# Kernel optimization log

Hardware: AMD Instinct MI355X
Metric: run time of the kernel (lower is better)

## Reference

```python
import jax, jax.numpy as jnp
import numpy as np

N_E = 1024
E_DIM = 64
BETA = 0.25


def setup_inputs() -> dict:
    key = jax.random.key(0)
    k1, k2 = jax.random.split(key)
    z = jax.random.normal(k1, (16, E_DIM, 64, 64), dtype=jnp.float32)
    # torch init: uniform(-1/n_e, 1/n_e)
    emb_w = jax.random.uniform(k2, (N_E, E_DIM), dtype=jnp.float32,
                               minval=-1.0 / N_E, maxval=1.0 / N_E)
    return {"z": z, "emb_w": emb_w}


def reference(z, emb_w):
    bt, ch, h, w = z.shape
    # (B, C, H, W) -> (B, H, W, C) -> (N, e_dim)
    z_perm = jnp.transpose(z, (0, 2, 3, 1))
    z_flat = z_perm.reshape(-1, ch)  # (N, e_dim)

    # squared euclidean distances: (N, n_e)
    distances = (jnp.sum(z_flat ** 2, axis=1, keepdims=True)
                 + jnp.sum(emb_w ** 2, axis=1)
                 - 2.0 * jnp.matmul(z_flat, emb_w.T))
    min_idx = jnp.argmin(distances, axis=1)  # (N,)

    min_encodings = jax.nn.one_hot(min_idx, N_E, dtype=z.dtype)  # (N, n_e)

    # gather codebook vectors (same math as one_hot @ emb_w)
    z_q = emb_w[min_idx].reshape(bt, h, w, ch)
    z_q = jnp.transpose(z_q, (0, 3, 1, 2))  # (B, C, H, W)

    commitment_loss = BETA * jnp.mean((jax.lax.stop_gradient(z_q) - z) ** 2)
    loss = commitment_loss

    # straight-through estimator
    z_q_st = z + jax.lax.stop_gradient(z_q - z)

    avg_probs = jnp.mean(min_encodings, axis=0)
    perplexity = jnp.exp(-jnp.sum(avg_probs * jnp.log(avg_probs + 1e-10)))

    min_encoding_indices = min_idx.reshape(bt, h, w)
    return loss, z_q_st, perplexity, min_encodings, min_encoding_indices
```

## Files before the change

### kernel.cpp

```cpp
#include <hip/hip_runtime.h>
#include <math.h>

#define NPOS   65536
#define NE     1024
#define EDIM   64
#define HW     4096
#define BETA   0.25

#define OUT_LOSS 0LL
#define OUT_ZQ   1LL
#define OUT_PERP 4194305LL
#define OUT_ENC  4194306LL
#define OUT_IDX  71303170LL

#define POSB 128
#define JT   128

__device__ __forceinline__ float pairwise_sum_sq64(const float v[64]) {
#pragma clang fp contract(off)
    float r[8];
#pragma unroll
    for (int k = 0; k < 8; ++k) r[k] = v[k] * v[k];
#pragma unroll
    for (int i = 8; i < 64; i += 8) {
#pragma unroll
        for (int k = 0; k < 8; ++k) {
            float s = v[i + k] * v[i + k];
            r[k] = r[k] + s;
        }
    }
    return ((r[0] + r[1]) + (r[2] + r[3])) + ((r[4] + r[5]) + (r[6] + r[7]));
}

__global__ void vq_prep(const float* __restrict__ emb, float* __restrict__ enorm,
                        float* __restrict__ embT, int* __restrict__ counts,
                        double* __restrict__ lacc) {
    int t = blockIdx.x * 256 + threadIdx.x;
    if (t < NE) {
        float v[64];
#pragma unroll
        for (int c = 0; c < 64; ++c) v[c] = emb[t * 64 + c];
        enorm[t] = pairwise_sum_sq64(v);
#pragma unroll
        for (int c = 0; c < 64; ++c) embT[c * NE + t] = v[c];
        counts[t] = 0;
    }
    if (t == 0) *lacc = 0.0;
}

__global__ __launch_bounds__(256, 4)
void vq_main(const float* __restrict__ z, const float* __restrict__ emb,
             const float* __restrict__ embT, const float* __restrict__ enorm,
             int* __restrict__ counts, double* __restrict__ lacc,
             float* __restrict__ out) {
    __shared__ float z_lds[64 * POSB];
    __shared__ float e_lds[64 * JT];
    __shared__ float enorm_lds[NE];
    __shared__ float szn_lds[POSB];
    __shared__ float run_d[POSB];
    __shared__ int   run_j[POSB];

    const int tid   = threadIdx.x;
    const int tpos  = tid >> 4;
    const int tcode = tid & 15;
    const int n0    = blockIdx.x * POSB;
    const int b     = n0 >> 12;
    const int hw0   = n0 & 4095;
    const int zbase = b * (64 * HW) + hw0;

#pragma unroll
    for (int it = 0; it < 8; ++it) {
        const int idx4 = it * 256 + tid;
        const int c    = idx4 >> 5;
        const int p4   = idx4 & 31;
        const float4 v = *(const float4*)(z + zbase + c * HW + p4 * 4);
        *(float4*)(&z_lds[c * POSB + p4 * 4]) = v;
    }
#pragma unroll
    for (int it = 0; it < 4; ++it) enorm_lds[it * 256 + tid] = enorm[it * 256 + tid];
    if (tid < POSB) { run_d[tid] = 3.4e38f; run_j[tid] = 0; }
    __syncthreads();

    if (tid < POSB) {
#pragma clang fp contract(off)
        float r[8];
#pragma unroll
        for (int k = 0; k < 8; ++k) { float x = z_lds[k * POSB + tid]; r[k] = x * x; }
#pragma unroll
        for (int i = 8; i < 64; i += 8) {
#pragma unroll
            for (int k = 0; k < 8; ++k) {
                float x = z_lds[(i + k) * POSB + tid];
                float s = x * x;
                r[k] = r[k] + s;
            }
        }
        szn_lds[tid] = ((r[0] + r[1]) + (r[2] + r[3])) + ((r[4] + r[5]) + (r[6] + r[7]));
    }
    __syncthreads();

    for (int jo = 0; jo < 8; ++jo) {
        const int j0 = jo * JT;

#pragma unroll
        for (int it = 0; it < 8; ++it) {
            const int idx4 = it * 256 + tid;
            const int c    = idx4 >> 5;
            const int q4   = idx4 & 31;
            const float4 v = *(const float4*)(embT + c * NE + j0 + q4 * 4);
            *(float4*)(&e_lds[c * JT + q4 * 4]) = v;
        }
        __syncthreads();

        float acc[8][8];
#pragma unroll
        for (int i = 0; i < 8; ++i)
#pragma unroll
            for (int u = 0; u < 8; ++u) acc[i][u] = 0.0f;

#pragma unroll 2
        for (int c = 0; c < 64; ++c) {
            const float4 za = *(const float4*)(&z_lds[c * POSB + tpos * 8]);
            const float4 zb = *(const float4*)(&z_lds[c * POSB + tpos * 8 + 4]);
            const float4 ea = *(const float4*)(&e_lds[c * JT + tcode * 4]);
            const float4 eb = *(const float4*)(&e_lds[c * JT + 64 + tcode * 4]);
            const float zf[8] = {za.x, za.y, za.z, za.w, zb.x, zb.y, zb.z, zb.w};
            const float ef[8] = {ea.x, ea.y, ea.z, ea.w, eb.x, eb.y, eb.z, eb.w};
#pragma unroll
            for (int i = 0; i < 8; ++i)
#pragma unroll
                for (int u = 0; u < 8; ++u)
                    acc[i][u] = fmaf(zf[i], ef[u], acc[i][u]);
        }

#pragma unroll
        for (int i = 0; i < 8; ++i) {
            const int p = tpos * 8 + i;
            const float sz = szn_lds[p];
            float bd = 3.4e38f;
            int   bj = 0;
#pragma unroll
            for (int u = 0; u < 4; ++u) {
                const int j = j0 + tcode * 4 + u;
                const float dj = (sz + enorm_lds[j]) - 2.0f * acc[i][u];
                if (dj < bd) { bd = dj; bj = j; }
            }
#pragma unroll
            for (int u = 0; u < 4; ++u) {
                const int j = j0 + 64 + tcode * 4 + u;
                const float dj = (sz + enorm_lds[j]) - 2.0f * acc[i][4 + u];
                if (dj < bd) { bd = dj; bj = j; }
            }
#pragma unroll
            for (int m = 1; m < 16; m <<= 1) {
                const float od = __shfl_xor(bd, m, 64);
                const int   oj = __shfl_xor(bj, m, 64);
                if (od < bd || (od == bd && oj < bj)) { bd = od; bj = oj; }
            }
            if (tcode == 0) {
                if (bd < run_d[p]) { run_d[p] = bd; run_j[p] = bj; }
            }
        }
        __syncthreads();
    }

    if (tid < POSB) {
        const int j = run_j[tid];
        atomicAdd(&counts[j], 1);
        out[OUT_IDX + n0 + tid] = (float)j;
        out[OUT_ENC + (long long)(n0 + tid) * NE + j] = 1.0f;
    }

    {
        const int pos = tid & 127;
        const int half = tid >> 7;
        const int myj = run_j[pos];
        double acc2 = 0.0;
#pragma unroll
        for (int k = 0; k < 32; ++k) {
            const int c = half * 32 + k;
            const float zc = z_lds[c * POSB + pos];
            const float ec = emb[myj * 64 + c];
            const float t  = __fsub_rn(ec, zc);
            const float o  = __fadd_rn(zc, t);
            out[OUT_ZQ + (long long)b * (64LL * HW) + (long long)c * HW + hw0 + pos] = o;
            const float s = __fmul_rn(t, t);
            acc2 += (double)s;
        }
#pragma unroll
        for (int off = 32; off > 0; off >>= 1) acc2 += __shfl_down(acc2, off);
        if ((tid & 63) == 0) atomicAdd(lacc, acc2);
    }
}

__global__ void vq_finalize(const int* __restrict__ counts,
                            const double* __restrict__ lacc,
                            float* __restrict__ out) {
    __shared__ float red[1024];
    const int t = threadIdx.x;
    const float p = (float)counts[t] * (1.0f / 65536.0f);
    const float term = p * logf(p + 1e-10f);
    red[t] = term;
    __syncthreads();
    for (int s = 512; s > 0; s >>= 1) {
        if (t < s) red[t] += red[t + s];
        __syncthreads();
    }
    if (t == 0) {
        out[OUT_PERP] = expf(-red[0]);
        out[OUT_LOSS] = (float)(BETA * (*lacc / 4194304.0));
    }
}

extern "C" void kernel_launch(void* const* d_in, const int* in_sizes, int n_in,
                              void* d_out, int out_size, void* d_ws, size_t ws_size,
                              hipStream_t stream) {
    const float* z   = (const float*)d_in[0];
    const float* emb = (const float*)d_in[1];
    float* out = (float*)d_out;

    double* lacc  = (double*)d_ws;
    int*    cnts  = (int*)((char*)d_ws + 16);
    float*  enorm = (float*)((char*)d_ws + 16 + NE * sizeof(int));
    float*  embT  = (float*)((char*)d_ws + 16 + NE * sizeof(int) + NE * sizeof(float));

    hipMemsetAsync(out + OUT_ENC, 0, (size_t)NPOS * NE * sizeof(float), stream);

    vq_prep<<<4, 256, 0, stream>>>(emb, enorm, embT, cnts, lacc);
    vq_main<<<512, 256, 0, stream>>>(z, emb, embT, enorm, cnts, lacc, out);
    vq_finalize<<<1, 1024, 0, stream>>>(cnts, lacc, out);
}
```

Measured before the change: 202.5 us.

## Fuse one-hot encoding write into main kernel and enlarge per-thread register tile

Drops the separate memset of the 256MB one-hot output and has the main kernel write every one-hot row directly, with zeros and the single one together as float2 stores. Block size is halved to 128 threads and each thread now handles 16 positions by 8 codes, keeping running minima and position norms in registers instead of LDS. This removes one full pass over the large output and some LDS traffic. In exchange the one-hot writes are serialized over 128 rows per block, and register pressure is higher with a single block allowed per CU by the launch bounds, which may cut occupancy.

```diff
diff --git a/kernel.cpp b/kernel.cpp
--- a/kernel.cpp
+++ b/kernel.cpp
@@ -48,7 +48,7 @@
     if (t == 0) *lacc = 0.0;
 }
 
-__global__ __launch_bounds__(256, 4)
+__global__ __launch_bounds__(128, 1)
 void vq_main(const float* __restrict__ z, const float* __restrict__ emb,
              const float* __restrict__ embT, const float* __restrict__ enorm,
              int* __restrict__ counts, double* __restrict__ lacc,
@@ -57,31 +57,29 @@
     __shared__ float e_lds[64 * JT];
     __shared__ float enorm_lds[NE];
     __shared__ float szn_lds[POSB];
-    __shared__ float run_d[POSB];
-    __shared__ int   run_j[POSB];
-
-    const int tid   = threadIdx.x;
-    const int tpos  = tid >> 4;
-    const int tcode = tid & 15;
-    const int n0    = blockIdx.x * POSB;
-    const int b     = n0 >> 12;
-    const int hw0   = n0 & 4095;
+    __shared__ int   run_j_lds[POSB];
+
+    const int tid = threadIdx.x;
+    const int T   = tid >> 4;
+    const int tc  = tid & 15;
+    const int n0  = blockIdx.x * POSB;
+    const int b   = n0 >> 12;
+    const int hw0 = n0 & 4095;
     const int zbase = b * (64 * HW) + hw0;
 
 #pragma unroll
-    for (int it = 0; it < 8; ++it) {
-        const int idx4 = it * 256 + tid;
+    for (int it = 0; it < 16; ++it) {
+        const int idx4 = it * 128 + tid;
         const int c    = idx4 >> 5;
         const int p4   = idx4 & 31;
         const float4 v = *(const float4*)(z + zbase + c * HW + p4 * 4);
         *(float4*)(&z_lds[c * POSB + p4 * 4]) = v;
     }
 #pragma unroll
-    for (int it = 0; it < 4; ++it) enorm_lds[it * 256 + tid] = enorm[it * 256 + tid];
-    if (tid < POSB) { run_d[tid] = 3.4e38f; run_j[tid] = 0; }
-    __syncthreads();
-
-    if (tid < POSB) {
+    for (int it = 0; it < 8; ++it) enorm_lds[it * 128 + tid] = enorm[it * 128 + tid];
+    __syncthreads();
+
+    {
 #pragma clang fp contract(off)
         float r[8];
 #pragma unroll
@@ -99,12 +97,24 @@
     }
     __syncthreads();
 
+    float my_szn[16];
+#pragma unroll
+    for (int pc = 0; pc < 4; ++pc) {
+        const float4 s4 = *(const float4*)(&szn_lds[pc * 32 + T * 4]);
+        my_szn[pc * 4 + 0] = s4.x; my_szn[pc * 4 + 1] = s4.y;
+        my_szn[pc * 4 + 2] = s4.z; my_szn[pc * 4 + 3] = s4.w;
+    }
+    float run_d[16];
+    int   run_j[16];
+#pragma unroll
+    for (int p = 0; p < 16; ++p) { run_d[p] = 3.4e38f; run_j[p] = 0; }
+
     for (int jo = 0; jo < 8; ++jo) {
         const int j0 = jo * JT;
 
 #pragma unroll
-        for (int it = 0; it < 8; ++it) {
-            const int idx4 = it * 256 + tid;
+        for (int it = 0; it < 16; ++it) {
+            const int idx4 = it * 128 + tid;
             const int c    = idx4 >> 5;
             const int q4   = idx4 & 31;
             const float4 v = *(const float4*)(embT + c * NE + j0 + q4 * 4);
@@ -112,43 +122,50 @@
         }
         __syncthreads();
 
-        float acc[8][8];
-#pragma unroll
-        for (int i = 0; i < 8; ++i)
-#pragma unroll
-            for (int u = 0; u < 8; ++u) acc[i][u] = 0.0f;
+        float acc[16][8];
+#pragma unroll
+        for (int p = 0; p < 16; ++p)
+#pragma unroll
+            for (int u = 0; u < 8; ++u) acc[p][u] = 0.0f;
 
 #pragma unroll 2
         for (int c = 0; c < 64; ++c) {
-            const float4 za = *(const float4*)(&z_lds[c * POSB + tpos * 8]);
-            const float4 zb = *(const float4*)(&z_lds[c * POSB + tpos * 8 + 4]);
-            const float4 ea = *(const float4*)(&e_lds[c * JT + tcode * 4]);
-            const float4 eb = *(const float4*)(&e_lds[c * JT + 64 + tcode * 4]);
-            const float zf[8] = {za.x, za.y, za.z, za.w, zb.x, zb.y, zb.z, zb.w};
+            float zf[16];
+#pragma unroll
+            for (int pc = 0; pc < 4; ++pc) {
+                const float4 v = *(const float4*)(&z_lds[c * POSB + pc * 32 + T * 4]);
+                zf[pc * 4 + 0] = v.x; zf[pc * 4 + 1] = v.y;
+                zf[pc * 4 + 2] = v.z; zf[pc * 4 + 3] = v.w;
+            }
+            const float4 ea = *(const float4*)(&e_lds[c * JT + tc * 4]);
+            const float4 eb = *(const float4*)(&e_lds[c * JT + 64 + tc * 4]);
             const float ef[8] = {ea.x, ea.y, ea.z, ea.w, eb.x, eb.y, eb.z, eb.w};
 #pragma unroll
-            for (int i = 0; i < 8; ++i)
+            for (int p = 0; p < 16; ++p)
 #pragma unroll
                 for (int u = 0; u < 8; ++u)
-                    acc[i][u] = fmaf(zf[i], ef[u], acc[i][u]);
-        }
-
-#pragma unroll
-        for (int i = 0; i < 8; ++i) {
-            const int p = tpos * 8 + i;
-            const float sz = szn_lds[p];
+                    acc[p][u] = fmaf(zf[p], ef[u], acc[p][u]);
+        }
+
+        const float4 enA = *(const float4*)(&enorm_lds[j0 + tc * 4]);
+        const float4 enB = *(const float4*)(&enorm_lds[j0 + 64 + tc * 4]);
+        const float enAf[4] = {enA.x, enA.y, enA.z, enA.w};
+        const float enBf[4] = {enB.x, enB.y, enB.z, enB.w};
+#pragma unroll
+        for (int p = 0; p < 16; ++p) {
+            const float sz = my_szn[p];
             float bd = 3.4e38f;
             int   bj = 0;
 #pragma unroll
             for (int u = 0; u < 4; ++u) {
-                const int j = j0 + tcode * 4 + u;
-                const float dj = (sz + enorm_lds[j]) - 2.0f * acc[i][u];
+                const int j = j0 + tc * 4 + u;
+                const float dj = (sz + enAf[u]) - 2.0f * acc[p][u];
                 if (dj < bd) { bd = dj; bj = j; }
             }
 #pragma unroll
             for (int u = 0; u < 4; ++u) {
-                const int j = j0 + 64 + tcode * 4 + u;
-                const float dj = (sz + enorm_lds[j]) - 2.0f * acc[i][4 + u];
+                const int j = j0 + 64 + tc * 4 + u;
+                const float dj = (sz + enBf[u]) - 2.0f * acc[p][4 + u];
                 if (dj < bd) { bd = dj; bj = j; }
             }
 #pragma unroll
@@ -157,39 +174,56 @@
                 const int   oj = __shfl_xor(bj, m, 64);
                 if (od < bd || (od == bd && oj < bj)) { bd = od; bj = oj; }
             }
-            if (tcode == 0) {
-                if (bd < run_d[p]) { run_d[p] = bd; run_j[p] = bj; }
-            }
+            if (bd < run_d[p]) { run_d[p] = bd; run_j[p] = bj; }
         }
         __syncthreads();
     }
 
-    if (tid < POSB) {
-        const int j = run_j[tid];
-        atomicAdd(&counts[j], 1);
-        out[OUT_IDX + n0 + tid] = (float)j;
-        out[OUT_ENC + (long long)(n0 + tid) * NE + j] = 1.0f;
-    }
+    if (tc == 0) {
+#pragma unroll
+        for (int pc = 0; pc < 4; ++pc)
+#pragma unroll
+            for (int i = 0; i < 4; ++i)
+                run_j_lds[pc * 32 + T * 4 + i] = run_j[pc * 4 + i];
+    }
+    __syncthreads();
+
+    const int myj = run_j_lds[tid];
+    atomicAdd(&counts[myj], 1);
+    out[OUT_IDX + n0 + tid] = (float)myj;
 
     {
-        const int pos = tid & 127;
-        const int half = tid >> 7;
-        const int myj = run_j[pos];
         double acc2 = 0.0;
-#pragma unroll
-        for (int k = 0; k < 32; ++k) {
-            const int c = half * 32 + k;
-            const float zc = z_lds[c * POSB + pos];
+#pragma unroll 8
+        for (int c = 0; c < 64; ++c) {
+            const float zc = z_lds[c * POSB + tid];
             const float ec = emb[myj * 64 + c];
             const float t  = __fsub_rn(ec, zc);
             const float o  = __fadd_rn(zc, t);
-            out[OUT_ZQ + (long long)b * (64LL * HW) + (long long)c * HW + hw0 + pos] = o;
+            out[OUT_ZQ + (long long)b * (64LL * HW) + (long long)c * HW + hw0 + tid] = o;
             const float s = __fmul_rn(t, t);
             acc2 += (double)s;
         }
 #pragma unroll
         for (int off = 32; off > 0; off >>= 1) acc2 += __shfl_down(acc2, off);
         if ((tid & 63) == 0) atomicAdd(lacc, acc2);
+    }
+
+    {
+        float2* __restrict__ enc2 = (float2*)(out + OUT_ENC);
+        for (int r = 0; r < POSB; ++r) {
+            const int ir = run_j_lds[r];
+            const long long rowb = (long long)(n0 + r) * 512;
+#pragma unroll
+            for (int q = 0; q < 4; ++q) {
+                const int g  = q * 128 + tid;
+                const int c0 = g * 2;
+                float2 v;
+                v.x = (c0     == ir) ? 1.0f : 0.0f;
+                v.y = (c0 + 1 == ir) ? 1.0f : 0.0f;
+                enc2[rowb + g] = v;
+            }
+        }
     }
 }
 
@@ -224,9 +258,7 @@
     float*  enorm = (float*)((char*)d_ws + 16 + NE * sizeof(int));
     float*  embT  = (float*)((char*)d_ws + 16 + NE * sizeof(int) + NE * sizeof(float));
 
-    hipMemsetAsync(out + OUT_ENC, 0, (size_t)NPOS * NE * sizeof(float), stream);
-
     vq_prep<<<4, 256, 0, stream>>>(emb, enorm, embT, cnts, lacc);
-    vq_main<<<512, 256, 0, stream>>>(z, emb, embT, enorm, cnts, lacc, out);
+    vq_main<<<512, 128, 0, stream>>>(z, emb, embT, enorm, cnts, lacc, out);
     vq_finalize<<<1, 1024, 0, stream>>>(cnts, lacc, out);
 }
```

New measurement: 245.8 us. 21.4% more time.

## Fuse one-hot zeroing into main kernel and shrink tiles to 64x64

Applied to the files above, without the earlier changes.

Removes the separate 256MB memset of the one-hot encodings output and has each block zero its own rows inside the distance loop, so those stores overlap the distance compute. Tiles shrink to 64 positions by 64 codes with a 4x4 per-thread accumulator, the grid doubles to 1024 blocks, and running argmin state moves from LDS into registers with a single shuffle reduction at the end. A threadfence orders the zero stores before the final 1.0 writes. The smaller register tile lowers arithmetic intensity per LDS load, and the zero-fill now shares bandwidth with the main kernel.

```diff
diff --git a/kernel.cpp b/kernel.cpp
--- a/kernel.cpp
+++ b/kernel.cpp
@@ -3,7 +3,6 @@
 
 #define NPOS   65536
 #define NE     1024
-#define EDIM   64
 #define HW     4096
 #define BETA   0.25
 
@@ -13,8 +12,8 @@
 #define OUT_ENC  4194306LL
 #define OUT_IDX  71303170LL
 
-#define POSB 128
-#define JT   128
+#define POSB 64
+#define JT   64
 
 __device__ __forceinline__ float pairwise_sum_sq64(const float v[64]) {
 #pragma clang fp contract(off)
@@ -55,30 +54,28 @@
              float* __restrict__ out) {
     __shared__ float z_lds[64 * POSB];
     __shared__ float e_lds[64 * JT];
-    __shared__ float enorm_lds[NE];
+    __shared__ float en_lds[NE];
     __shared__ float szn_lds[POSB];
-    __shared__ float run_d[POSB];
-    __shared__ int   run_j[POSB];
-
-    const int tid   = threadIdx.x;
-    const int tpos  = tid >> 4;
-    const int tcode = tid & 15;
-    const int n0    = blockIdx.x * POSB;
-    const int b     = n0 >> 12;
-    const int hw0   = n0 & 4095;
+    __shared__ int   run_j_lds[POSB];
+
+    const int tid = threadIdx.x;
+    const int tc  = tid & 15;
+    const int T   = tid >> 4;
+    const int n0  = blockIdx.x * POSB;
+    const int b   = n0 >> 12;
+    const int hw0 = n0 & 4095;
     const int zbase = b * (64 * HW) + hw0;
 
 #pragma unroll
-    for (int it = 0; it < 8; ++it) {
+    for (int it = 0; it < 4; ++it) {
         const int idx4 = it * 256 + tid;
-        const int c    = idx4 >> 5;
-        const int p4   = idx4 & 31;
+        const int c    = idx4 >> 4;
+        const int p4   = idx4 & 15;
         const float4 v = *(const float4*)(z + zbase + c * HW + p4 * 4);
         *(float4*)(&z_lds[c * POSB + p4 * 4]) = v;
     }
 #pragma unroll
-    for (int it = 0; it < 4; ++it) enorm_lds[it * 256 + tid] = enorm[it * 256 + tid];
-    if (tid < POSB) { run_d[tid] = 3.4e38f; run_j[tid] = 0; }
+    for (int it = 0; it < 4; ++it) en_lds[it * 256 + tid] = enorm[it * 256 + tid];
     __syncthreads();
 
     if (tid < POSB) {
@@ -99,86 +96,104 @@
     }
     __syncthreads();
 
-    for (int jo = 0; jo < 8; ++jo) {
+    float msz[4];
+    {
+        const float4 s4 = *(const float4*)(&szn_lds[T * 4]);
+        msz[0] = s4.x; msz[1] = s4.y; msz[2] = s4.z; msz[3] = s4.w;
+    }
+    float run_d[4];
+    int   run_j[4];
+#pragma unroll
+    for (int i = 0; i < 4; ++i) { run_d[i] = 3.4e38f; run_j[i] = 0; }
+
+    float2* __restrict__ enc2 = (float2*)(out + OUT_ENC);
+    const long long encbase = (long long)n0 * 512;
+
+    for (int jo = 0; jo < 16; ++jo) {
         const int j0 = jo * JT;
 
 #pragma unroll
-        for (int it = 0; it < 8; ++it) {
+        for (int it = 0; it < 4; ++it) {
             const int idx4 = it * 256 + tid;
-            const int c    = idx4 >> 5;
-            const int q4   = idx4 & 31;
+            const int c    = idx4 >> 4;
+            const int q4   = idx4 & 15;
             const float4 v = *(const float4*)(embT + c * NE + j0 + q4 * 4);
             *(float4*)(&e_lds[c * JT + q4 * 4]) = v;
         }
         __syncthreads();
 
-        float acc[8][8];
-#pragma unroll
-        for (int i = 0; i < 8; ++i)
-#pragma unroll
-            for (int u = 0; u < 8; ++u) acc[i][u] = 0.0f;
-
-#pragma unroll 2
+        float acc[4][4];
+#pragma unroll
+        for (int i = 0; i < 4; ++i)
+#pragma unroll
+            for (int u = 0; u < 4; ++u) acc[i][u] = 0.0f;
+
+#pragma unroll 8
         for (int c = 0; c < 64; ++c) {
-            const float4 za = *(const float4*)(&z_lds[c * POSB + tpos * 8]);
-            const float4 zb = *(const float4*)(&z_lds[c * POSB + tpos * 8 + 4]);
-            const float4 ea = *(const float4*)(&e_lds[c * JT + tcode * 4]);
-            const float4 eb = *(const float4*)(&e_lds[c * JT + 64 + tcode * 4]);
-            const float zf[8] = {za.x, za.y, za.z, za.w, zb.x, zb.y, zb.z, zb.w};
-            const float ef[8] = {ea.x, ea.y, ea.z, ea.w, eb.x, eb.y, eb.z, eb.w};
-#pragma unroll
-            for (int i = 0; i < 8; ++i)
-#pragma unroll
-                for (int u = 0; u < 8; ++u)
-                    acc[i][u] = fmaf(zf[i], ef[u], acc[i][u]);
-        }
-
-#pragma unroll
-        for (int i = 0; i < 8; ++i) {
-            const int p = tpos * 8 + i;
-            const float sz = szn_lds[p];
-            float bd = 3.4e38f;
-            int   bj = 0;
-#pragma unroll
-            for (int u = 0; u < 4; ++u) {
-                const int j = j0 + tcode * 4 + u;
-                const float dj = (sz + enorm_lds[j]) - 2.0f * acc[i][u];
-                if (dj < bd) { bd = dj; bj = j; }
+            const float4 za = *(const float4*)(&z_lds[c * POSB + T * 4]);
+            const float4 ef = *(const float4*)(&e_lds[c * JT + tc * 4]);
+            const float zf[4] = {za.x, za.y, za.z, za.w};
+            const float ev[4] = {ef.x, ef.y, ef.z, ef.w};
+#pragma unroll
+            for (int i = 0; i < 4; ++i)
+#pragma unroll
+                for (int u = 0; u < 4; ++u)
+                    acc[i][u] = fmaf(zf[i], ev[u], acc[i][u]);
+        }
+
+        {
+            const float4 en4 = *(const float4*)(&en_lds[j0 + tc * 4]);
+            const float env[4] = {en4.x, en4.y, en4.z, en4.w};
+#pragma unroll
+            for (int i = 0; i < 4; ++i) {
+#pragma unroll
+                for (int u = 0; u < 4; ++u) {
+                    const float dj = (msz[i] + env[u]) - 2.0f * acc[i][u];
+                    if (dj < run_d[i]) { run_d[i] = dj; run_j[i] = j0 + tc * 4 + u; }
+                }
             }
-#pragma unroll
-            for (int u = 0; u < 4; ++u) {
-                const int j = j0 + 64 + tcode * 4 + u;
-                const float dj = (sz + enorm_lds[j]) - 2.0f * acc[i][4 + u];
-                if (dj < bd) { bd = dj; bj = j; }
-            }
-#pragma unroll
-            for (int m = 1; m < 16; m <<= 1) {
-                const float od = __shfl_xor(bd, m, 64);
-                const int   oj = __shfl_xor(bj, m, 64);
-                if (od < bd || (od == bd && oj < bj)) { bd = od; bj = oj; }
-            }
-            if (tcode == 0) {
-                if (bd < run_d[p]) { run_d[p] = bd; run_j[p] = bj; }
-            }
-        }
+        }
+
+#pragma unroll
+        for (int k = 0; k < 8; ++k) {
+            const float2 zero2 = {0.0f, 0.0f};
+            enc2[encbase + jo * 2048 + k * 256 + tid] = zero2;
+        }
+
         __syncthreads();
     }
 
+    __threadfence();
+
+#pragma unroll
+    for (int i = 0; i < 4; ++i) {
+        float bd = run_d[i];
+        int   bj = run_j[i];
+#pragma unroll
+        for (int m = 1; m < 16; m <<= 1) {
+            const float od = __shfl_xor(bd, m, 64);
+            const int   oj = __shfl_xor(bj, m, 64);
+            if (od < bd || (od == bd && oj < bj)) { bd = od; bj = oj; }
+        }
+        if (tc == 0) run_j_lds[T * 4 + i] = bj;
+    }
+    __syncthreads();
+
     if (tid < POSB) {
-        const int j = run_j[tid];
+        const int j = run_j_lds[tid];
         atomicAdd(&counts[j], 1);
         out[OUT_IDX + n0 + tid] = (float)j;
         out[OUT_ENC + (long long)(n0 + tid) * NE + j] = 1.0f;
     }
 
     {
-        const int pos = tid & 127;
-        const int half = tid >> 7;
-        const int myj = run_j[pos];
+        const int pos = tid & 63;
+        const int cq  = tid >> 6;
+        const int myj = run_j_lds[pos];
         double acc2 = 0.0;
 #pragma unroll
-        for (int k = 0; k < 32; ++k) {
-            const int c = half * 32 + k;
+        for (int k = 0; k < 16; ++k) {
+            const int c = cq * 16 + k;
             const float zc = z_lds[c * POSB + pos];
             const float ec = emb[myj * 64 + c];
             const float t  = __fsub_rn(ec, zc);
@@ -224,9 +239,7 @@
     float*  enorm = (float*)((char*)d_ws + 16 + NE * sizeof(int));
     float*  embT  = (float*)((char*)d_ws + 16 + NE * sizeof(int) + NE * sizeof(float));
 
-    hipMemsetAsync(out + OUT_ENC, 0, (size_t)NPOS * NE * sizeof(float), stream);
-
     vq_prep<<<4, 256, 0, stream>>>(emb, enorm, embT, cnts, lacc);
-    vq_main<<<512, 256, 0, stream>>>(z, emb, embT, enorm, cnts, lacc, out);
+    vq_main<<<1024, 256, 0, stream>>>(z, emb, embT, enorm, cnts, lacc, out);
     vq_finalize<<<1, 1024, 0, stream>>>(cnts, lacc, out);
 }
```

Result: slower. 283.7 us (+40.1%).

## Fuse one-hot encoding write into main kernel and retile to 16 positions per block

Applied to the files above, without the earlier changes.

Drops the separate memset of the 256MB one-hot output. The main kernel now writes the whole encoding row itself, including zeros, with 64-bit nontemporal stores. Blocks shrink to 16 positions each and stream the whole codebook through double-buffered LDS in 4-channel chunks, with z read straight from global per wave, and the grid grows from 512 to 4096 blocks. This removes a full extra pass over the large output and spreads that write across many more blocks, at the cost of re-reading the codebook once per block.

```diff
diff --git a/kernel.cpp b/kernel.cpp
--- a/kernel.cpp
+++ b/kernel.cpp
@@ -3,7 +3,6 @@
 
 #define NPOS   65536
 #define NE     1024
-#define EDIM   64
 #define HW     4096
 #define BETA   0.25
 
@@ -12,9 +11,6 @@
 #define OUT_PERP 4194305LL
 #define OUT_ENC  4194306LL
 #define OUT_IDX  71303170LL
-
-#define POSB 128
-#define JT   128
 
 __device__ __forceinline__ float pairwise_sum_sq64(const float v[64]) {
 #pragma clang fp contract(off)
@@ -53,133 +49,144 @@
              const float* __restrict__ embT, const float* __restrict__ enorm,
              int* __restrict__ counts, double* __restrict__ lacc,
              float* __restrict__ out) {
-    __shared__ float z_lds[64 * POSB];
-    __shared__ float e_lds[64 * JT];
-    __shared__ float enorm_lds[NE];
-    __shared__ float szn_lds[POSB];
-    __shared__ float run_d[POSB];
-    __shared__ int   run_j[POSB];
-
-    const int tid   = threadIdx.x;
-    const int tpos  = tid >> 4;
-    const int tcode = tid & 15;
-    const int n0    = blockIdx.x * POSB;
-    const int b     = n0 >> 12;
-    const int hw0   = n0 & 4095;
+    __shared__ float e_lds[2][4 * NE];
+    __shared__ float en_lds[NE];
+    __shared__ float szn_lds[16];
+    __shared__ float cand_d[2][16];
+    __shared__ int   cand_j[2][16];
+    __shared__ int   runj[16];
+
+    const int tid  = threadIdx.x;
+    const int lane = tid & 63;
+    const int w    = tid >> 6;
+    const int wp   = w >> 1;
+    const int wc   = w & 1;
+    const int n0   = blockIdx.x * 16;
+    const int b    = n0 >> 12;
+    const int hw0  = n0 & 4095;
     const int zbase = b * (64 * HW) + hw0;
-
-#pragma unroll
-    for (int it = 0; it < 8; ++it) {
-        const int idx4 = it * 256 + tid;
-        const int c    = idx4 >> 5;
-        const int p4   = idx4 & 31;
-        const float4 v = *(const float4*)(z + zbase + c * HW + p4 * 4);
-        *(float4*)(&z_lds[c * POSB + p4 * 4]) = v;
-    }
-#pragma unroll
-    for (int it = 0; it < 4; ++it) enorm_lds[it * 256 + tid] = enorm[it * 256 + tid];
-    if (tid < POSB) { run_d[tid] = 3.4e38f; run_j[tid] = 0; }
-    __syncthreads();
-
-    if (tid < POSB) {
+    const int ebase = wc * 512 + lane * 8;
+
+#pragma unroll
+    for (int it = 0; it < 4; ++it) en_lds[it * 256 + tid] = enorm[it * 256 + tid];
+
+    if (tid < 16) {
 #pragma clang fp contract(off)
         float r[8];
 #pragma unroll
-        for (int k = 0; k < 8; ++k) { float x = z_lds[k * POSB + tid]; r[k] = x * x; }
+        for (int k = 0; k < 8; ++k) { float x = z[zbase + k * HW + tid]; r[k] = x * x; }
 #pragma unroll
         for (int i = 8; i < 64; i += 8) {
 #pragma unroll
             for (int k = 0; k < 8; ++k) {
-                float x = z_lds[(i + k) * POSB + tid];
+                float x = z[zbase + (i + k) * HW + tid];
                 float s = x * x;
                 r[k] = r[k] + s;
             }
         }
         szn_lds[tid] = ((r[0] + r[1]) + (r[2] + r[3])) + ((r[4] + r[5]) + (r[6] + r[7]));
     }
-    __syncthreads();
-
-    for (int jo = 0; jo < 8; ++jo) {
-        const int j0 = jo * JT;
-
-#pragma unroll
-        for (int it = 0; it < 8; ++it) {
-            const int idx4 = it * 256 + tid;
-            const int c    = idx4 >> 5;
-            const int q4   = idx4 & 31;
-            const float4 v = *(const float4*)(embT + c * NE + j0 + q4 * 4);
-            *(float4*)(&e_lds[c * JT + q4 * 4]) = v;
-        }
-        __syncthreads();
-
-        float acc[8][8];
-#pragma unroll
-        for (int i = 0; i < 8; ++i)
-#pragma unroll
-            for (int u = 0; u < 8; ++u) acc[i][u] = 0.0f;
-
-#pragma unroll 2
-        for (int c = 0; c < 64; ++c) {
-            const float4 za = *(const float4*)(&z_lds[c * POSB + tpos * 8]);
-            const float4 zb = *(const float4*)(&z_lds[c * POSB + tpos * 8 + 4]);
-            const float4 ea = *(const float4*)(&e_lds[c * JT + tcode * 4]);
-            const float4 eb = *(const float4*)(&e_lds[c * JT + 64 + tcode * 4]);
-            const float zf[8] = {za.x, za.y, za.z, za.w, zb.x, zb.y, zb.z, zb.w};
-            const float ef[8] = {ea.x, ea.y, ea.z, ea.w, eb.x, eb.y, eb.z, eb.w};
-#pragma unroll
-            for (int i = 0; i < 8; ++i)
-#pragma unroll
-                for (int u = 0; u < 8; ++u)
-                    acc[i][u] = fmaf(zf[i], ef[u], acc[i][u]);
-        }
-
-#pragma unroll
-        for (int i = 0; i < 8; ++i) {
-            const int p = tpos * 8 + i;
-            const float sz = szn_lds[p];
-            float bd = 3.4e38f;
-            int   bj = 0;
-#pragma unroll
-            for (int u = 0; u < 4; ++u) {
-                const int j = j0 + tcode * 4 + u;
-                const float dj = (sz + enorm_lds[j]) - 2.0f * acc[i][u];
-                if (dj < bd) { bd = dj; bj = j; }
-            }
-#pragma unroll
-            for (int u = 0; u < 4; ++u) {
-                const int j = j0 + 64 + tcode * 4 + u;
-                const float dj = (sz + enorm_lds[j]) - 2.0f * acc[i][4 + u];
-                if (dj < bd) { bd = dj; bj = j; }
-            }
-#pragma unroll
-            for (int m = 1; m < 16; m <<= 1) {
-                const float od = __shfl_xor(bd, m, 64);
-                const int   oj = __shfl_xor(bj, m, 64);
-                if (od < bd || (od == bd && oj < bj)) { bd = od; bj = oj; }
-            }
-            if (tcode == 0) {
-                if (bd < run_d[p]) { run_d[p] = bd; run_j[p] = bj; }
-            }
-        }
-        __syncthreads();
-    }
-
-    if (tid < POSB) {
-        const int j = run_j[tid];
-        atomicAdd(&counts[j], 1);
-        out[OUT_IDX + n0 + tid] = (float)j;
-        out[OUT_ENC + (long long)(n0 + tid) * NE + j] = 1.0f;
-    }
+
+#pragma unroll
+    for (int it = 0; it < 4; ++it) {
+        const int idx4 = it * 256 + tid;
+        const int cc   = idx4 >> 8;
+        const int q4   = idx4 & 255;
+        const float4 v = *(const float4*)(embT + cc * NE + q4 * 4);
+        *(float4*)(&e_lds[0][cc * NE + q4 * 4]) = v;
+    }
+    __syncthreads();
+
+    const int zoffu = __builtin_amdgcn_readfirstlane(zbase + wp * 8);
+    const float* __restrict__ zw = z + zoffu;
+
+    float acc[8][8];
+#pragma unroll
+    for (int p = 0; p < 8; ++p)
+#pragma unroll
+        for (int u = 0; u < 8; ++u) acc[p][u] = 0.0f;
+
+#define VQ_BODY(CUR, NXT, CH)                                                   \
+    do {                                                                        \
+        if ((CH) + 1 < 16) {                                                    \
+            const int c0n = ((CH) + 1) * 4;                                     \
+            _Pragma("unroll")                                                   \
+            for (int it = 0; it < 4; ++it) {                                    \
+                const int idx4 = it * 256 + tid;                                \
+                const int cc   = idx4 >> 8;                                     \
+                const int q4   = idx4 & 255;                                    \
+                const float4 v = *(const float4*)(embT + (c0n + cc) * NE + q4 * 4); \
+                *(float4*)(&e_lds[NXT][cc * NE + q4 * 4]) = v;                  \
+            }                                                                   \
+        }                                                                       \
+        {                                                                       \
+            const float* __restrict__ zwc = zw + (CH) * 4 * HW;                 \
+            float zc[4][8];                                                     \
+            _Pragma("unroll")                                                   \
+            for (int cc = 0; cc < 4; ++cc)                                      \
+                _Pragma("unroll")                                               \
+                for (int p = 0; p < 8; ++p) zc[cc][p] = zwc[cc * HW + p];       \
+            _Pragma("unroll")                                                   \
+            for (int cc = 0; cc < 4; ++cc) {                                    \
+                const float4 ea = *(const float4*)(&e_lds[CUR][cc * NE + ebase]);     \
+                const float4 eb = *(const float4*)(&e_lds[CUR][cc * NE + ebase + 4]); \
+                const float ef[8] = {ea.x, ea.y, ea.z, ea.w, eb.x, eb.y, eb.z, eb.w}; \
+                _Pragma("unroll")                                               \
+                for (int p = 0; p < 8; ++p)                                     \
+                    _Pragma("unroll")                                           \
+                    for (int u = 0; u < 8; ++u)                                 \
+                        acc[p][u] = fmaf(zc[cc][p], ef[u], acc[p][u]);          \
+            }                                                                   \
+        }                                                                       \
+        __syncthreads();                                                        \
+    } while (0)
+
+    for (int ch = 0; ch < 16; ch += 2) {
+        VQ_BODY(0, 1, ch);
+        VQ_BODY(1, 0, ch + 1);
+    }
+#undef VQ_BODY
+
+#pragma unroll
+    for (int p = 0; p < 8; ++p) {
+        const float sz = szn_lds[wp * 8 + p];
+        float bd = 3.4e38f;
+        int   bj = 0;
+#pragma unroll
+        for (int u = 0; u < 8; ++u) {
+            const int j = ebase + u;
+            const float dj = (sz + en_lds[j]) - 2.0f * acc[p][u];
+            if (dj < bd) { bd = dj; bj = j; }
+        }
+#pragma unroll
+        for (int m = 1; m < 64; m <<= 1) {
+            const float od = __shfl_xor(bd, m, 64);
+            const int   oj = __shfl_xor(bj, m, 64);
+            if (od < bd || (od == bd && oj < bj)) { bd = od; bj = oj; }
+        }
+        if (lane == 0) { cand_d[wc][wp * 8 + p] = bd; cand_j[wc][wp * 8 + p] = bj; }
+    }
+    __syncthreads();
+
+    if (tid < 16) {
+        const float d0 = cand_d[0][tid];
+        const float d1 = cand_d[1][tid];
+        const int   jf = (d1 < d0) ? cand_j[1][tid] : cand_j[0][tid];
+        runj[tid] = jf;
+        atomicAdd(&counts[jf], 1);
+        out[OUT_IDX + n0 + tid] = (float)jf;
+    }
+    __syncthreads();
 
     {
-        const int pos = tid & 127;
-        const int half = tid >> 7;
-        const int myj = run_j[pos];
+        const int pos  = tid & 15;
+        const int cseg = tid >> 4;
+        const int myj  = runj[pos];
         double acc2 = 0.0;
 #pragma unroll
-        for (int k = 0; k < 32; ++k) {
-            const int c = half * 32 + k;
-            const float zc = z_lds[c * POSB + pos];
+        for (int k = 0; k < 4; ++k) {
+            const int c = cseg * 4 + k;
+            const float zc = z[zbase + c * HW + pos];
             const float ec = emb[myj * 64 + c];
             const float t  = __fsub_rn(ec, zc);
             const float o  = __fadd_rn(zc, t);
@@ -189,7 +196,25 @@
         }
 #pragma unroll
         for (int off = 32; off > 0; off >>= 1) acc2 += __shfl_down(acc2, off);
-        if ((tid & 63) == 0) atomicAdd(lacc, acc2);
+        if (lane == 0) atomicAdd(lacc, acc2);
+    }
+
+    {
+        unsigned long long* __restrict__ enc8 =
+            (unsigned long long*)(out + OUT_ENC);
+        const long long encb = (long long)n0 * 512;
+#pragma unroll
+        for (int i = 0; i < 32; ++i) {
+            const int g   = i * 256 + tid;
+            const int row = g >> 9;
+            const int col = g & 511;
+            const int jr  = runj[row];
+            const int c0  = col * 2;
+            unsigned long long v = 0ULL;
+            if (c0 == jr)     v = 0x3f800000ULL;
+            if (c0 + 1 == jr) v = 0x3f800000ULL << 32;
+            __builtin_nontemporal_store(v, &enc8[encb + (long long)row * 512 + col]);
+        }
     }
 }
 
@@ -224,9 +249,7 @@
     float*  enorm = (float*)((char*)d_ws + 16 + NE * sizeof(int));
     float*  embT  = (float*)((char*)d_ws + 16 + NE * sizeof(int) + NE * sizeof(float));
 
-    hipMemsetAsync(out + OUT_ENC, 0, (size_t)NPOS * NE * sizeof(float), stream);
-
     vq_prep<<<4, 256, 0, stream>>>(emb, enorm, embT, cnts, lacc);
-    vq_main<<<512, 256, 0, stream>>>(z, emb, embT, enorm, cnts, lacc, out);
+    vq_main<<<4096, 256, 0, stream>>>(z, emb, embT, enorm, cnts, lacc, out);
     vq_finalize<<<1, 1024, 0, stream>>>(cnts, lacc, out);
 }
```

Result: slower. 268.1 us (+32.4%).
